# Kernel tuning notes

Hardware: AMD Instinct MI355X
Metric: run time of the kernel (lower is better)

The kernel has to match this reference:

```python
import jax, jax.numpy as jnp
import numpy as np

N_NODES = 30000
N_EDGES = 480000
NUM_RELS = 8
NUM_BASES = 4
F_IN = 32
HID = 64
HEADS = 4
N_CLASSES = 3
NEG_SLOPE = 0.2


def setup_inputs() -> dict:
    key = jax.random.key(0)
    ks = jax.random.split(key, 16)
    s = lambda k, shape: jax.random.normal(k, shape, jnp.float32) * 0.1
    return {
        'x': jax.random.normal(ks[0], (N_NODES, F_IN), jnp.float32),
        'edge_index': jax.random.randint(ks[1], (2, N_EDGES), 0, N_NODES),
        'edge_type': jax.random.randint(ks[2], (N_EDGES,), 0, NUM_RELS),
        # RGCN layer 1 (basis decomposition)
        'basis1': s(ks[3], (NUM_BASES, F_IN, HID)),
        'comp1': s(ks[4], (NUM_RELS, NUM_BASES)),
        'root1': s(ks[5], (F_IN, HID)),
        'brg1': jnp.zeros((HID,), jnp.float32),
        # GAT layer 1 (concat=True -> out dim HEADS*HID)
        'Wg1': s(ks[6], (HID, HEADS * HID)),
        'atts1': s(ks[7], (HEADS, HID)),
        'attd1': s(ks[8], (HEADS, HID)),
        'bg1': jnp.zeros((HEADS * HID,), jnp.float32),
        # RGCN layer 2
        'basis2': s(ks[9], (NUM_BASES, HEADS * HID, HID)),
        'comp2': s(ks[10], (NUM_RELS, NUM_BASES)),
        'root2': s(ks[11], (HEADS * HID, HID)),
        'brg2': jnp.zeros((HID,), jnp.float32),
        # GAT layer 2 (concat=False -> mean over heads, out dim N_CLASSES)
        'Wg2': s(ks[12], (HID, HEADS * N_CLASSES)),
        'atts2': s(ks[13], (HEADS, N_CLASSES)),
        'attd2': s(ks[14], (HEADS, N_CLASSES)),
        'bg2': jnp.zeros((N_CLASSES,), jnp.float32),
    }


def _rgcn(x, src, dst, etype, basis, comp, root, bias):
    # RGCNConv with basis decomposition, aggr='mean' (PyG default), root weight + bias.
    n = x.shape[0]
    w = jnp.einsum('rb,bio->rio', comp, basis)          # [R, in, out]
    xr = jnp.einsum('ni,rio->nro', x, w)                # [N, R, out]
    msg = xr[src, etype]                                # [E, out] gather per edge
    agg = jax.ops.segment_sum(msg, dst, num_segments=n)
    deg = jax.ops.segment_sum(jnp.ones((src.shape[0],), x.dtype), dst, num_segments=n)
    agg = agg / jnp.maximum(deg, 1.0)[:, None]          # mean over incoming edges
    return agg + x @ root + bias


def _gat(x, src, dst, w, att_s, att_d, bias, concat):
    # GATConv with self-loops (PyG default add_self_loops=True).
    n = x.shape[0]
    heads, c = att_s.shape
    loop = jnp.arange(n)
    s2 = jnp.concatenate([src, loop])
    d2 = jnp.concatenate([dst, loop])
    h = (x @ w).reshape(n, heads, c)                    # [N, H, C]
    a_s = jnp.einsum('nhc,hc->nh', h, att_s)
    a_d = jnp.einsum('nhc,hc->nh', h, att_d)
    e = jax.nn.leaky_relu(a_s[s2] + a_d[d2], NEG_SLOPE)  # [E2, H]
    emax = jax.ops.segment_max(e, d2, num_segments=n)    # stable softmax over in-edges
    p = jnp.exp(e - emax[d2])
    denom = jax.ops.segment_sum(p, d2, num_segments=n)
    alpha = p / denom[d2]
    out = jax.ops.segment_sum(alpha[:, :, None] * h[s2], d2, num_segments=n)  # [N, H, C]
    if concat:
        return out.reshape(n, heads * c) + bias
    return out.mean(axis=1) + bias


def reference(x, edge_index, edge_type, basis1, comp1, root1, brg1, Wg1, atts1, attd1, bg1, basis2, comp2, root2, brg2, Wg2, atts2, attd2, bg2):
    src, dst = edge_index[0], edge_index[1]
    h = jax.nn.elu(_rgcn(x, src, dst, edge_type, basis1, comp1, root1, brg1))
    h = jax.nn.elu(_gat(h, src, dst, Wg1, atts1, attd1, bg1, True))
    h = jax.nn.elu(_rgcn(h, src, dst, edge_type, basis2, comp2, root2, brg2))
    h = _gat(h, src, dst, Wg2, atts2, attd2, bg2, False)   # [N, n_classes]
    return jnp.tanh(h.mean(axis=1, keepdims=True))         # [N, 1]
```

## Files before the change

kernel.cpp:

```cpp
#include <hip/hip_runtime.h>
#include <cstdint>
#include <cstddef>

#define NN 30000
#define NE 480000

typedef __attribute__((ext_vector_type(8))) short short8v;
typedef __attribute__((ext_vector_type(4))) float f32x4;

__device__ __forceinline__ float leakyf(float x){ return x > 0.f ? x : 0.2f * x; }
__device__ __forceinline__ float eluf(float x){ return x > 0.f ? x : expm1f(x); }

__device__ __forceinline__ float bf2f(unsigned short u){
  return __uint_as_float(((unsigned)u) << 16);
}
__device__ __forceinline__ unsigned short f2bf(float f){
  unsigned x = __float_as_uint(f);
  unsigned r = (x + 0x7FFFu + ((x >> 16) & 1u)) >> 16;
  return (unsigned short)r;
}

struct F4 { float x, y, z, w; };

__device__ __forceinline__ F4 ld4(const float* p){
  float4 v = *(const float4*)p;
  return F4{v.x, v.y, v.z, v.w};
}

__device__ __forceinline__ float4 redeg16(float4 v){
  v.x += __shfl_xor(v.x, 16); v.y += __shfl_xor(v.y, 16);
  v.z += __shfl_xor(v.z, 16); v.w += __shfl_xor(v.w, 16);
  v.x += __shfl_xor(v.x, 32); v.y += __shfl_xor(v.y, 32);
  v.z += __shfl_xor(v.z, 32); v.w += __shfl_xor(v.w, 32);
  return v;
}


__global__ void zero2_kernel(int* __restrict__ a, int* __restrict__ b, int n){
  int i = blockIdx.x * blockDim.x + threadIdx.x;
  if (i < n){ a[i] = 0; b[i] = 0; }
}

__global__ void count_kernel(const int* __restrict__ dst, int* __restrict__ deg, int E){
  int i = blockIdx.x * blockDim.x + threadIdx.x;
  if (i < E) atomicAdd(&deg[dst[i]], 1);
}

__global__ void scan1_kernel(const int* __restrict__ deg, int* __restrict__ offs,
                             int* __restrict__ bsum){
  __shared__ int sh[256];
  int blk = blockIdx.x, t = threadIdx.x, i = blk * 256 + t;
  int v = (i < NN) ? deg[i] : 0;
  sh[t] = v; __syncthreads();
  for (int o = 1; o < 256; o <<= 1){
    int tv = (t >= o) ? sh[t - o] : 0;
    __syncthreads();
    sh[t] += tv;
    __syncthreads();
  }
  if (i < NN) offs[i + 1] = sh[t];
  if (t == 255) bsum[blk] = sh[255];
}

__global__ void scan2_kernel(int* __restrict__ bsum, int nb){
  __shared__ int sh[256];
  int t = threadIdx.x;
  int v = (t < nb) ? bsum[t] : 0;
  sh[t] = v; __syncthreads();
  for (int o = 1; o < 256; o <<= 1){
    int tv = (t >= o) ? sh[t - o] : 0;
    __syncthreads();
    sh[t] += tv;
    __syncthreads();
  }
  if (t < nb) bsum[t] = sh[t];
}

__global__ void scan3_kernel(const int* __restrict__ bsum, int* __restrict__ offs){
  int i = blockIdx.x * 256 + threadIdx.x;
  if (i == 0) offs[0] = 0;
  if (i < NN){
    int blk = i >> 8;
    int add = blk ? bsum[blk - 1] : 0;
    offs[i + 1] += add;
  }
}

__global__ void scatter_kernel(const int* __restrict__ src, const int* __restrict__ dst,
                               const int* __restrict__ et, const int* __restrict__ offs,
                               int* __restrict__ cursor, int* __restrict__ csr_src,
                               int* __restrict__ csr_et, int E){
  int i = blockIdx.x * blockDim.x + threadIdx.x;
  if (i < E){
    int d = dst[i];
    int pos = offs[d] + atomicAdd(&cursor[d], 1);
    csr_src[pos] = src[i];
    csr_et[pos]  = et[i];
  }
}


__global__ void wcat2_kernel(const float* __restrict__ basis2, const float* __restrict__ root2,
                             float* __restrict__ Wcat){
  int idx = blockIdx.x * 256 + threadIdx.x;
  if (idx >= 256 * 384) return;
  int k = idx / 384, col = idx - k * 384;
  float v = 0.f;
  if (col < 256){
    int b = col >> 6, c = col & 63;
    v = basis2[((size_t)b * 256 + k) * 64 + c];
  } else if (col < 320){
    v = root2[(size_t)k * 64 + (col - 256)];
  }
  Wcat[idx] = v;
}

__global__ void packB_kernel(const float* __restrict__ W, int ldw, int ksteps, int total,
                             unsigned short* __restrict__ Bhi, unsigned short* __restrict__ Blo){
  int idx = blockIdx.x * 256 + threadIdx.x;
  if (idx >= total) return;
  int lane = idx & 63;
  int rest = idx >> 6;
  int ks = rest % ksteps;
  int nf16 = rest / ksteps;
  int col = nf16 * 16 + (lane & 15);
  int kbase = ks * 32 + ((lane >> 4) << 3);
  size_t obase = (size_t)idx * 8;
  #pragma unroll
  for (int j = 0; j < 8; j++){
    float v = W[(size_t)(kbase + j) * ldw + col];
    unsigned short h = f2bf(v);
    float res = v - bf2f(h);
    Bhi[obase + j] = h;
    Blo[obase + j] = f2bf(res);
  }
}

__global__ void wa_kernel(const float* __restrict__ Wg1, const float* __restrict__ atts1,
                          const float* __restrict__ attd1, float* __restrict__ wa_s,
                          float* __restrict__ wa_d){
  int t = threadIdx.x;
  int k = t >> 2, h = t & 3;
  float s = 0.f, d = 0.f;
  const float* wr = Wg1 + (size_t)k * 256 + h * 64;
  const float* pa = atts1 + h * 64;
  const float* pb = attd1 + h * 64;
  #pragma unroll 8
  for (int c = 0; c < 64; c++){ s += wr[c] * pa[c]; d += wr[c] * pb[c]; }
  wa_s[k * 4 + h] = s;
  wa_d[k * 4 + h] = d;
}

__global__ void logits_kernel(const float* __restrict__ h1, const float* __restrict__ wa_s,
                              const float* __restrict__ wa_d, float* __restrict__ as_,
                              float* __restrict__ ad_){
  __shared__ float ws[256], wd[256];
  int t = threadIdx.x;
  ws[t] = wa_s[t];
  wd[t] = wa_d[t];
  __syncthreads();
  int idx = blockIdx.x * 256 + t;
  int n = idx >> 2, h = idx & 3;
  if (n >= NN) return;
  float s = 0.f, d = 0.f;
  const float* hr = h1 + (size_t)n * 64;
  #pragma unroll 4
  for (int k4 = 0; k4 < 16; k4++){
    float4 hv = *(const float4*)(hr + k4 * 4);
    s += hv.x * ws[(k4*4+0)*4+h] + hv.y * ws[(k4*4+1)*4+h]
       + hv.z * ws[(k4*4+2)*4+h] + hv.w * ws[(k4*4+3)*4+h];
    d += hv.x * wd[(k4*4+0)*4+h] + hv.y * wd[(k4*4+1)*4+h]
       + hv.z * wd[(k4*4+2)*4+h] + hv.w * wd[(k4*4+3)*4+h];
  }
  as_[n * 4 + h] = s;
  ad_[n * 4 + h] = d;
}


__global__ void agg1_kernel(const float* __restrict__ x, const float* __restrict__ comp,
                            const int* __restrict__ offs, const int* __restrict__ csr_src,
                            const int* __restrict__ csr_et, float* __restrict__ agg){
  int wid  = (blockIdx.x * blockDim.x + threadIdx.x) >> 6;
  int lane = threadIdx.x & 63;
  if (wid >= NN) return;
  int q = lane & 15, eg = lane >> 4;
  int c2 = q * 2;
  int n0 = offs[wid], n1 = offs[wid + 1];
  float a00 = 0.f, a01 = 0.f, a10 = 0.f, a11 = 0.f;
  float a20 = 0.f, a21 = 0.f, a30 = 0.f, a31 = 0.f;
  for (int k = n0 + eg; k < n1; k += 4){
    int s = csr_src[k], e = csr_et[k];
    float2 v = *(const float2*)(x + (size_t)s * 32 + c2);
    F4 cp = ld4(comp + (size_t)e * 4);
    a00 += cp.x * v.x; a01 += cp.x * v.y;
    a10 += cp.y * v.x; a11 += cp.y * v.y;
    a20 += cp.z * v.x; a21 += cp.z * v.y;
    a30 += cp.w * v.x; a31 += cp.w * v.y;
  }
  #pragma unroll
  for (int o = 16; o < 64; o <<= 1){
    a00 += __shfl_xor(a00, o); a01 += __shfl_xor(a01, o);
    a10 += __shfl_xor(a10, o); a11 += __shfl_xor(a11, o);
    a20 += __shfl_xor(a20, o); a21 += __shfl_xor(a21, o);
    a30 += __shfl_xor(a30, o); a31 += __shfl_xor(a31, o);
  }
  int dg = n1 - n0;
  float sc = 1.f / (float)(dg > 0 ? dg : 1);
  if (lane < 16){
    float* ar = agg + (size_t)wid * 128 + c2;
    *(float2*)(ar)      = make_float2(a00 * sc, a01 * sc);
    *(float2*)(ar + 32) = make_float2(a10 * sc, a11 * sc);
    *(float2*)(ar + 64) = make_float2(a20 * sc, a21 * sc);
    *(float2*)(ar + 96) = make_float2(a30 * sc, a31 * sc);
  }
}


template<int RPT, bool ELU>
__global__ __launch_bounds__(256) void gemmT_kernel(
    const float* __restrict__ A1, int lda1, int K1,
    const float* __restrict__ W1, int ldw1,
    const float* __restrict__ A2, int lda2, int K2,
    const float* __restrict__ W2, int ldw2,
    const float* __restrict__ bias,
    float* __restrict__ Y, int ldy,
    int nrows, int acgoff, int wcgoff)
{
  __shared__ float At[32][RPT * 16 + 4];
  __shared__ float Wl[32][68];
  int t = threadIdx.x;
  int tc = t & 15, tr = t >> 4;
  int cg = blockIdx.x;
  int nbase = blockIdx.y * (RPT * 16);
  float acc[RPT][4];
  #pragma unroll
  for (int j = 0; j < RPT; j++)
    #pragma unroll
    for (int i = 0; i < 4; i++) acc[j][i] = 0.f;

  for (int seg = 0; seg < 2; seg++){
    const float* A = seg ? A2 : A1;
    const float* W = seg ? W2 : W1;
    int lda = seg ? lda2 : lda1;
    int ldw = seg ? ldw2 : ldw1;
    int K   = seg ? K2 : K1;
    if (A == nullptr || K <= 0) continue;
    A += (size_t)cg * acgoff;
    W += (size_t)cg * wcgoff;
    for (int k0 = 0; k0 < K; k0 += 32){
      #pragma unroll
      for (int i = 0; i < 2; i++){
        int e = i * 256 + t;
        int kk = e >> 4, c4 = (e & 15) << 2;
        float4 v = make_float4(0.f, 0.f, 0.f, 0.f);
        if (k0 + kk < K) v = *(const float4*)(W + (size_t)(k0 + kk) * ldw + c4);
        *(float4*)&Wl[kk][c4] = v;
      }
      #pragma unroll
      for (int i = 0; i < RPT / 2; i++){
        int e = i * 256 + t;
        int r = e >> 3, c4 = (e & 7) << 2;
        int n = nbase + r;
        float4 v = make_float4(0.f, 0.f, 0.f, 0.f);
        if (n < nrows && k0 + c4 < K) v = *(const float4*)(A + (size_t)n * lda + k0 + c4);
        At[c4 + 0][r] = v.x;
        At[c4 + 1][r] = v.y;
        At[c4 + 2][r] = v.z;
        At[c4 + 3][r] = v.w;
      }
      __syncthreads();
      #pragma unroll 4
      for (int k = 0; k < 32; k++){
        float4 wv = *(const float4*)&Wl[k][tc * 4];
        const float* pw = (const float*)&wv;
        #pragma unroll
        for (int jj = 0; jj < RPT / 4; jj++){
          float4 av = *(const float4*)&At[k][tr * RPT + jj * 4];
          const float* pa = (const float*)&av;
          #pragma unroll
          for (int j = 0; j < 4; j++)
            #pragma unroll
            for (int i = 0; i < 4; i++)
              acc[jj * 4 + j][i] = fmaf(pa[j], pw[i], acc[jj * 4 + j][i]);
        }
      }
      __syncthreads();
    }
  }

  float b0 = 0.f, b1 = 0.f, b2 = 0.f, b3 = 0.f;
  if (bias){
    b0 = bias[cg * 64 + tc * 4 + 0];
    b1 = bias[cg * 64 + tc * 4 + 1];
    b2 = bias[cg * 64 + tc * 4 + 2];
    b3 = bias[cg * 64 + tc * 4 + 3];
  }
  #pragma unroll
  for (int j = 0; j < RPT; j++){
    int n = nbase + tr * RPT + j;
    if (n < nrows){
      float y0 = acc[j][0] + b0, y1 = acc[j][1] + b1;
      float y2 = acc[j][2] + b2, y3 = acc[j][3] + b3;
      if (ELU){ y0 = eluf(y0); y1 = eluf(y1); y2 = eluf(y2); y3 = eluf(y3); }
      *(float4*)(Y + (size_t)n * ldy + cg * 64 + tc * 4) = make_float4(y0, y1, y2, y3);
    }
  }
}


template<int KSTEPS, bool ELU, bool BIAS>
__global__ __launch_bounds__(256) void gemm_mfma_kernel(
    const float* __restrict__ A, int lda, int acgoff,
    const unsigned short* __restrict__ Bhi, const unsigned short* __restrict__ Blo,
    const float* __restrict__ bias, float* __restrict__ Y, int ldy)
{
  int t = threadIdx.x;
  int lane = t & 63, wv = t >> 6;
  int cg = blockIdx.x;
  int mbase = blockIdx.y * 256 + wv * 64;
  int fr = lane & 15;
  int ksub = (lane >> 4) << 3;
  const float* Ab = A + (size_t)cg * acgoff;
  f32x4 acc[4][4];
  #pragma unroll
  for (int mi = 0; mi < 4; mi++)
    #pragma unroll
    for (int ni = 0; ni < 4; ni++)
      acc[mi][ni] = (f32x4){0.f, 0.f, 0.f, 0.f};

  #pragma unroll
  for (int ks = 0; ks < KSTEPS; ks++){
    short8v ahi[4], alo[4];
    #pragma unroll
    for (int mi = 0; mi < 4; mi++){
      int r = mbase + mi * 16 + fr;
      float av[8];
      if (r < NN){
        float4 p0 = *(const float4*)(Ab + (size_t)r * lda + ks * 32 + ksub);
        float4 p1 = *(const float4*)(Ab + (size_t)r * lda + ks * 32 + ksub + 4);
        av[0] = p0.x; av[1] = p0.y; av[2] = p0.z; av[3] = p0.w;
        av[4] = p1.x; av[5] = p1.y; av[6] = p1.z; av[7] = p1.w;
      } else {
        #pragma unroll
        for (int j = 0; j < 8; j++) av[j] = 0.f;
      }
      #pragma unroll
      for (int j = 0; j < 8; j++){
        unsigned short h = f2bf(av[j]);
        float res = av[j] - bf2f(h);
        ahi[mi][j] = (short)h;
        alo[mi][j] = (short)f2bf(res);
      }
    }
    #pragma unroll
    for (int ni = 0; ni < 4; ni++){
      size_t boff = ((((size_t)(cg * 4 + ni)) * KSTEPS + ks) * 64 + lane) * 8;
      short8v bh = *(const short8v*)(Bhi + boff);
      short8v bl = *(const short8v*)(Blo + boff);
      #pragma unroll
      for (int mi = 0; mi < 4; mi++){
        acc[mi][ni] = __builtin_amdgcn_mfma_f32_16x16x32_bf16(ahi[mi], bh, acc[mi][ni], 0, 0, 0);
        acc[mi][ni] = __builtin_amdgcn_mfma_f32_16x16x32_bf16(ahi[mi], bl, acc[mi][ni], 0, 0, 0);
        acc[mi][ni] = __builtin_amdgcn_mfma_f32_16x16x32_bf16(alo[mi], bh, acc[mi][ni], 0, 0, 0);
      }
    }
  }
  int crow = (lane >> 4) << 2;
  #pragma unroll
  for (int mi = 0; mi < 4; mi++){
    #pragma unroll
    for (int reg = 0; reg < 4; reg++){
      int r = mbase + mi * 16 + crow + reg;
      if (r < NN){
        #pragma unroll
        for (int ni = 0; ni < 4; ni++){
          float y = acc[mi][ni][reg];
          if (BIAS) y += bias[cg * 64 + ni * 16 + fr];
          if (ELU)  y = eluf(y);
          Y[(size_t)r * ldy + cg * 64 + ni * 16 + fr] = y;
        }
      }
    }
  }
}


__global__ __launch_bounds__(256) void gemm_l3_fused_kernel(
    const float* __restrict__ A,
    const unsigned short* __restrict__ Bhi, const unsigned short* __restrict__ Blo,
    const float* __restrict__ comp2,
    unsigned short* __restrict__ xr, float* __restrict__ rootb)
{
  int t = threadIdx.x;
  int lane = t & 63, wv = t >> 6;
  int of = blockIdx.x;
  int mbase = blockIdx.y * 64 + wv * 16;
  int fr = lane & 15;
  int ksub = (lane >> 4) << 3;
  f32x4 acc[5];
  #pragma unroll
  for (int b = 0; b < 5; b++) acc[b] = (f32x4){0.f, 0.f, 0.f, 0.f};

  int ar = mbase + fr;
  bool arok = (ar < NN);
  for (int ks = 0; ks < 8; ks++){
    float av[8];
    if (arok){
      float4 p0 = *(const float4*)(A + (size_t)ar * 256 + ks * 32 + ksub);
      float4 p1 = *(const float4*)(A + (size_t)ar * 256 + ks * 32 + ksub + 4);
      av[0] = p0.x; av[1] = p0.y; av[2] = p0.z; av[3] = p0.w;
      av[4] = p1.x; av[5] = p1.y; av[6] = p1.z; av[7] = p1.w;
    } else {
      #pragma unroll
      for (int j = 0; j < 8; j++) av[j] = 0.f;
    }
    short8v ahi, alo;
    #pragma unroll
    for (int j = 0; j < 8; j++){
      unsigned short h = f2bf(av[j]);
      float res = av[j] - bf2f(h);
      ahi[j] = (short)h;
      alo[j] = (short)f2bf(res);
    }
    #pragma unroll
    for (int b = 0; b < 5; b++){
      int nig = b * 4 + of;
      size_t boff = (((size_t)nig * 8 + ks) * 64 + lane) * 8;
      short8v bh = *(const short8v*)(Bhi + boff);
      short8v bl = *(const short8v*)(Blo + boff);
      acc[b] = __builtin_amdgcn_mfma_f32_16x16x32_bf16(ahi, bh, acc[b], 0, 0, 0);
      acc[b] = __builtin_amdgcn_mfma_f32_16x16x32_bf16(ahi, bl, acc[b], 0, 0, 0);
      acc[b] = __builtin_amdgcn_mfma_f32_16x16x32_bf16(alo, bh, acc[b], 0, 0, 0);
    }
  }

  float cp[32];
  #pragma unroll
  for (int i = 0; i < 32; i++) cp[i] = comp2[i];
  int crow = (lane >> 4) << 2;
  int col = of * 16 + fr;
  #pragma unroll
  for (int reg = 0; reg < 4; reg++){
    int r = mbase + crow + reg;
    if (r >= NN) continue;
    float b0 = acc[0][reg], b1 = acc[1][reg], b2 = acc[2][reg], b3 = acc[3][reg];
    rootb[(size_t)r * 64 + col] = acc[4][reg];
    #pragma unroll
    for (int rr = 0; rr < 8; rr++){
      float m = cp[rr*4+0]*b0 + cp[rr*4+1]*b1 + cp[rr*4+2]*b2 + cp[rr*4+3]*b3;
      xr[((size_t)r * 8 + rr) * 64 + col] = f2bf(m);
    }
  }
}


__global__ void gat1_agg_kernel(const float* __restrict__ h1, const float* __restrict__ as_,
                                const float* __restrict__ ad_, const int* __restrict__ offs,
                                const int* __restrict__ csr_src, float* __restrict__ aggG){
  int wid  = (blockIdx.x * blockDim.x + threadIdx.x) >> 6;
  int lane = threadIdx.x & 63;
  if (wid >= NN) return;
  int n0 = offs[wid], n1 = offs[wid + 1];
  int h = lane & 3;
  float adn_s = ad_[wid * 4 + h];
  float m = leakyf(as_[wid * 4 + h] + adn_s);
  for (int k = n0 + (lane >> 2); k < n1; k += 16){
    int s = csr_src[k];
    m = fmaxf(m, leakyf(as_[s * 4 + h] + adn_s));
  }
  #pragma unroll
  for (int o = 4; o < 64; o <<= 1) m = fmaxf(m, __shfl_xor(m, o));
  float m0 = __shfl(m, 0), m1 = __shfl(m, 1), m2 = __shfl(m, 2), m3 = __shfl(m, 3);
  int q = lane & 15, eg = lane >> 4;
  F4 adn = ld4(ad_ + (size_t)wid * 4);
  float den0 = 0.f, den1 = 0.f, den2 = 0.f, den3 = 0.f;
  float4 ac0 = make_float4(0.f,0.f,0.f,0.f), ac1 = ac0, ac2 = ac0, ac3 = ac0;
  for (int k = n0 + eg; k < n1; k += 4){
    int s = csr_src[k];
    F4 a = ld4(as_ + (size_t)s * 4);
    float p0 = expf(leakyf(a.x + adn.x) - m0);
    float p1 = expf(leakyf(a.y + adn.y) - m1);
    float p2 = expf(leakyf(a.z + adn.z) - m2);
    float p3 = expf(leakyf(a.w + adn.w) - m3);
    den0 += p0; den1 += p1; den2 += p2; den3 += p3;
    float4 v = *(const float4*)(h1 + (size_t)s * 64 + q * 4);
    ac0.x += p0*v.x; ac0.y += p0*v.y; ac0.z += p0*v.z; ac0.w += p0*v.w;
    ac1.x += p1*v.x; ac1.y += p1*v.y; ac1.z += p1*v.z; ac1.w += p1*v.w;
    ac2.x += p2*v.x; ac2.y += p2*v.y; ac2.z += p2*v.z; ac2.w += p2*v.w;
    ac3.x += p3*v.x; ac3.y += p3*v.y; ac3.z += p3*v.z; ac3.w += p3*v.w;
  }
  #pragma unroll
  for (int o = 16; o < 64; o <<= 1){
    den0 += __shfl_xor(den0, o); den1 += __shfl_xor(den1, o);
    den2 += __shfl_xor(den2, o); den3 += __shfl_xor(den3, o);
  }
  ac0 = redeg16(ac0); ac1 = redeg16(ac1); ac2 = redeg16(ac2); ac3 = redeg16(ac3);
  F4 asn = ld4(as_ + (size_t)wid * 4);
  float ps0 = expf(leakyf(asn.x + adn.x) - m0);
  float ps1 = expf(leakyf(asn.y + adn.y) - m1);
  float ps2 = expf(leakyf(asn.z + adn.z) - m2);
  float ps3 = expf(leakyf(asn.w + adn.w) - m3);
  if (lane < 16){
    float4 v = *(const float4*)(h1 + (size_t)wid * 64 + q * 4);
    float i0 = 1.f / (den0 + ps0), i1 = 1.f / (den1 + ps1);
    float i2 = 1.f / (den2 + ps2), i3 = 1.f / (den3 + ps3);
    float* ag = aggG + (size_t)wid * 256 + q * 4;
    *(float4*)(ag)       = make_float4((ac0.x+ps0*v.x)*i0, (ac0.y+ps0*v.y)*i0, (ac0.z+ps0*v.z)*i0, (ac0.w+ps0*v.w)*i0);
    *(float4*)(ag + 64)  = make_float4((ac1.x+ps1*v.x)*i1, (ac1.y+ps1*v.y)*i1, (ac1.z+ps1*v.z)*i1, (ac1.w+ps1*v.w)*i1);
    *(float4*)(ag + 128) = make_float4((ac2.x+ps2*v.x)*i2, (ac2.y+ps2*v.y)*i2, (ac2.z+ps2*v.z)*i2, (ac2.w+ps2*v.w)*i2);
    *(float4*)(ag + 192) = make_float4((ac3.x+ps3*v.x)*i3, (ac3.y+ps3*v.y)*i3, (ac3.z+ps3*v.z)*i3, (ac3.w+ps3*v.w)*i3);
  }
}


__global__ void rgcn2_agg_kernel(const unsigned short* __restrict__ xr,
                                 const float* __restrict__ rootb,
                                 const float* __restrict__ bias, const int* __restrict__ offs,
                                 const int* __restrict__ csr_src, const int* __restrict__ csr_et,
                                 float* __restrict__ h3){
  int wid  = (blockIdx.x * blockDim.x + threadIdx.x) >> 6;
  int lane = threadIdx.x & 63;
  if (wid >= NN) return;
  int q = lane & 7, eg = lane >> 3;
  int n0 = offs[wid], n1 = offs[wid + 1];
  float a[8];
  #pragma unroll
  for (int j = 0; j < 8; j++) a[j] = 0.f;
  for (int k = n0 + eg; k < n1; k += 8){
    int s = csr_src[k], e = csr_et[k];
    short8v u = *(const short8v*)(xr + ((size_t)s * 8 + e) * 64 + q * 8);
    #pragma unroll
    for (int j = 0; j < 8; j++) a[j] += bf2f((unsigned short)u[j]);
  }
  #pragma unroll
  for (int o = 8; o < 64; o <<= 1){
    #pragma unroll
    for (int j = 0; j < 8; j++) a[j] += __shfl_xor(a[j], o);
  }
  int dg = n1 - n0;
  float sc = 1.f / (float)(dg > 0 ? dg : 1);
  if (lane < 8){
    const float* rb = rootb + (size_t)wid * 64 + q * 8;
    float4 r0 = *(const float4*)(rb);
    float4 r1 = *(const float4*)(rb + 4);
    float4 b0 = *(const float4*)(bias + q * 8);
    float4 b1 = *(const float4*)(bias + q * 8 + 4);
    float* hp = h3 + (size_t)wid * 64 + q * 8;
    *(float4*)(hp)     = make_float4(eluf(a[0]*sc + r0.x + b0.x), eluf(a[1]*sc + r0.y + b0.y),
                                     eluf(a[2]*sc + r0.z + b0.z), eluf(a[3]*sc + r0.w + b0.w));
    *(float4*)(hp + 4) = make_float4(eluf(a[4]*sc + r1.x + b1.x), eluf(a[5]*sc + r1.y + b1.y),
                                     eluf(a[6]*sc + r1.z + b1.z), eluf(a[7]*sc + r1.w + b1.w));
  }
}


__global__ void gat_lin2_kernel(const float* __restrict__ h, const float* __restrict__ W,
                                const float* __restrict__ atts, const float* __restrict__ attd,
                                float* __restrict__ hw, float* __restrict__ as_, float* __restrict__ ad_){
  int wid  = (blockIdx.x * blockDim.x + threadIdx.x) >> 6;
  int lane = threadIdx.x & 63;
  if (wid >= NN) return;
  float acc = 0.f;
  if (lane < 12){
    const float* hr = h + (size_t)wid * 64;
    const float* Wc = W + lane;
    #pragma unroll 8
    for (int i = 0; i < 64; i++) acc += hr[i] * Wc[(size_t)i * 12];
    hw[(size_t)wid * 12 + lane] = acc;
  }
  float ts = (lane < 12) ? acc * atts[lane] : 0.f;
  float td = (lane < 12) ? acc * attd[lane] : 0.f;
  int b = (lane < 4) ? lane * 3 : 0;
  float s0 = __shfl(ts, b) + __shfl(ts, b + 1) + __shfl(ts, b + 2);
  float d0 = __shfl(td, b) + __shfl(td, b + 1) + __shfl(td, b + 2);
  if (lane < 4){ as_[wid * 4 + lane] = s0; ad_[wid * 4 + lane] = d0; }
}

__global__ void gat2_final_kernel(const float* __restrict__ hw, const float* __restrict__ as_,
                                  const float* __restrict__ ad_, const float* __restrict__ bg2,
                                  const int* __restrict__ offs, const int* __restrict__ csr_src,
                                  float* __restrict__ out){
  int wid  = (blockIdx.x * blockDim.x + threadIdx.x) >> 6;
  int lane = threadIdx.x & 63;
  if (wid >= NN) return;
  int n0 = offs[wid], n1 = offs[wid + 1];
  F4 adn = ld4(ad_ + (size_t)wid * 4);
  F4 asn = ld4(as_ + (size_t)wid * 4);
  F4 es{leakyf(asn.x + adn.x), leakyf(asn.y + adn.y), leakyf(asn.z + adn.z), leakyf(asn.w + adn.w)};
  F4 m = es;
  for (int k = n0 + lane; k < n1; k += 64){
    int s = csr_src[k];
    F4 a = ld4(as_ + (size_t)s * 4);
    m.x = fmaxf(m.x, leakyf(a.x + adn.x));
    m.y = fmaxf(m.y, leakyf(a.y + adn.y));
    m.z = fmaxf(m.z, leakyf(a.z + adn.z));
    m.w = fmaxf(m.w, leakyf(a.w + adn.w));
  }
  #pragma unroll
  for (int o = 32; o; o >>= 1){
    m.x = fmaxf(m.x, __shfl_xor(m.x, o));
    m.y = fmaxf(m.y, __shfl_xor(m.y, o));
    m.z = fmaxf(m.z, __shfl_xor(m.z, o));
    m.w = fmaxf(m.w, __shfl_xor(m.w, o));
  }
  F4 ps{expf(es.x - m.x), expf(es.y - m.y), expf(es.z - m.z), expf(es.w - m.w)};
  float acc[12];
  #pragma unroll
  for (int j = 0; j < 12; j++) acc[j] = 0.f;
  F4 denp{0.f, 0.f, 0.f, 0.f};
  for (int k = n0 + lane; k < n1; k += 64){
    int s = csr_src[k];
    F4 a = ld4(as_ + (size_t)s * 4);
    F4 p{expf(leakyf(a.x + adn.x) - m.x), expf(leakyf(a.y + adn.y) - m.y),
         expf(leakyf(a.z + adn.z) - m.z), expf(leakyf(a.w + adn.w) - m.w)};
    denp.x += p.x; denp.y += p.y; denp.z += p.z; denp.w += p.w;
    const float* hb = hw + (size_t)s * 12;
    F4 h0 = ld4(hb), h1 = ld4(hb + 4), h2 = ld4(hb + 8);
    acc[0] += p.x * h0.x; acc[1]  += p.x * h0.y; acc[2]  += p.x * h0.z;
    acc[3] += p.y * h0.w; acc[4]  += p.y * h1.x; acc[5]  += p.y * h1.y;
    acc[6] += p.z * h1.z; acc[7]  += p.z * h1.w; acc[8]  += p.z * h2.x;
    acc[9] += p.w * h2.y; acc[10] += p.w * h2.z; acc[11] += p.w * h2.w;
  }
  #pragma unroll
  for (int o = 32; o; o >>= 1){
    denp.x += __shfl_xor(denp.x, o);
    denp.y += __shfl_xor(denp.y, o);
    denp.z += __shfl_xor(denp.z, o);
    denp.w += __shfl_xor(denp.w, o);
    #pragma unroll
    for (int j = 0; j < 12; j++) acc[j] += __shfl_xor(acc[j], o);
  }
  if (lane == 0){
    const float* hn = hw + (size_t)wid * 12;
    float dn[4]  = {denp.x + ps.x, denp.y + ps.y, denp.z + ps.z, denp.w + ps.w};
    float psv[4] = {ps.x, ps.y, ps.z, ps.w};
    float tot = 0.f;
    #pragma unroll
    for (int h_ = 0; h_ < 4; h_++){
      #pragma unroll
      for (int c = 0; c < 3; c++){
        float num = acc[h_ * 3 + c] + psv[h_] * hn[h_ * 3 + c];
        tot += num / dn[h_];
      }
    }
    tot = tot / 12.f + (bg2[0] + bg2[1] + bg2[2]) / 3.f;
    out[wid] = tanhf(tot);
  }
}


extern "C" void kernel_launch(void* const* d_in, const int* in_sizes, int n_in,
                              void* d_out, int out_size, void* d_ws, size_t ws_size,
                              hipStream_t stream){
  const float* x      = (const float*)d_in[0];
  const int*   ei     = (const int*)d_in[1];
  const int*   et     = (const int*)d_in[2];
  const float* basis1 = (const float*)d_in[3];
  const float* comp1  = (const float*)d_in[4];
  const float* root1  = (const float*)d_in[5];
  const float* brg1   = (const float*)d_in[6];
  const float* Wg1    = (const float*)d_in[7];
  const float* atts1  = (const float*)d_in[8];
  const float* attd1  = (const float*)d_in[9];
  const float* bg1    = (const float*)d_in[10];
  const float* basis2 = (const float*)d_in[11];
  const float* comp2  = (const float*)d_in[12];
  const float* root2  = (const float*)d_in[13];
  const float* brg2   = (const float*)d_in[14];
  const float* Wg2    = (const float*)d_in[15];
  const float* atts2  = (const float*)d_in[16];
  const float* attd2  = (const float*)d_in[17];
  const float* bg2    = (const float*)d_in[18];
  float* out = (float*)d_out;

  const int* src = ei;
  const int* dst = ei + NE;

  char* ws = (char*)d_ws;
  size_t off = 0;
  auto alloc = [&](size_t bytes) -> void* {
    void* p = ws + off;
    off = (off + bytes + 255) & ~(size_t)255;
    return p;
  };
  int*   deg     = (int*)alloc((size_t)NN * 4);
  int*   cursor  = (int*)alloc((size_t)NN * 4);
  int*   offs    = (int*)alloc((size_t)(NN + 1) * 4);
  int*   bsum    = (int*)alloc((size_t)256 * 4);
  int*   csr_src = (int*)alloc((size_t)NE * 4);
  int*   csr_et  = (int*)alloc((size_t)NE * 4);
  float* Wcat2   = (float*)alloc((size_t)256 * 384 * 4);
  unsigned short* Bhi2 = (unsigned short*)alloc((size_t)81920 * 2);
  unsigned short* Blo2 = (unsigned short*)alloc((size_t)81920 * 2);
  unsigned short* Bhi1 = (unsigned short*)alloc((size_t)16384 * 2);
  unsigned short* Blo1 = (unsigned short*)alloc((size_t)16384 * 2);
  float* wa_s    = (float*)alloc((size_t)256 * 4);
  float* wa_d    = (float*)alloc((size_t)256 * 4);
  float* h1      = (float*)alloc((size_t)NN * 64 * 4);
  float* h2      = (float*)alloc((size_t)NN * 256 * 4);
  float* h3      = (float*)alloc((size_t)NN * 64 * 4);
  float* hw2     = (float*)alloc((size_t)NN * 12 * 4);
  float* as1     = (float*)alloc((size_t)NN * 4 * 4);
  float* ad1     = (float*)alloc((size_t)NN * 4 * 4);
  float* as2     = (float*)alloc((size_t)NN * 4 * 4);
  float* ad2     = (float*)alloc((size_t)NN * 4 * 4);
  float* S       = (float*)alloc((size_t)NN * 384 * 4);
  float* agg1    = S;
  float* aggG    = S;
  unsigned short* xr = (unsigned short*)S;
  float* rootb   = S + (size_t)NN * 256;
  (void)ws_size; (void)n_in; (void)in_sizes; (void)out_size;

  const int BLK = 256;
  int gridN   = (NN + BLK - 1) / BLK;
  int gridE   = (NE + BLK - 1) / BLK;
  int gridW   = (NN + 3) / 4;
  int gridM64 = (NN + 63) / 64;
  int gridM256= (NN + 255) / 256;

  zero2_kernel<<<gridN, BLK, 0, stream>>>(deg, cursor, NN);
  count_kernel<<<gridE, BLK, 0, stream>>>(dst, deg, NE);
  wcat2_kernel<<<(256 * 384 + 255) / 256, BLK, 0, stream>>>(basis2, root2, Wcat2);
  packB_kernel<<<(10240 + 255) / 256, BLK, 0, stream>>>(Wcat2, 384, 8, 10240, Bhi2, Blo2);
  packB_kernel<<<(2048 + 255) / 256, BLK, 0, stream>>>(Wg1, 256, 2, 2048, Bhi1, Blo1);
  wa_kernel<<<1, BLK, 0, stream>>>(Wg1, atts1, attd1, wa_s, wa_d);
  scan1_kernel<<<gridN, BLK, 0, stream>>>(deg, offs, bsum);
  scan2_kernel<<<1, BLK, 0, stream>>>(bsum, gridN);
  scan3_kernel<<<gridN, BLK, 0, stream>>>(bsum, offs);
  scatter_kernel<<<gridE, BLK, 0, stream>>>(src, dst, et, offs, cursor, csr_src, csr_et, NE);

  agg1_kernel<<<gridW, BLK, 0, stream>>>(x, comp1, offs, csr_src, csr_et, agg1);
  gemmT_kernel<4, true><<<dim3(1, gridM64), BLK, 0, stream>>>(
      agg1, 128, 128, basis1, 64,
      x, 32, 32, root1, 64,
      brg1, h1, 64, NN, 0, 0);

  logits_kernel<<<(NN * 4 + 255) / 256, BLK, 0, stream>>>(h1, wa_s, wa_d, as1, ad1);
  gat1_agg_kernel<<<gridW, BLK, 0, stream>>>(h1, as1, ad1, offs, csr_src, aggG);
  gemm_mfma_kernel<2, true, true><<<dim3(4, gridM256), BLK, 0, stream>>>(
      aggG, 256, 64, Bhi1, Blo1, bg1, h2, 256);

  gemm_l3_fused_kernel<<<dim3(4, gridM64), BLK, 0, stream>>>(h2, Bhi2, Blo2, comp2, xr, rootb);
  rgcn2_agg_kernel<<<gridW, BLK, 0, stream>>>(xr, rootb, brg2, offs, csr_src, csr_et, h3);

  gat_lin2_kernel<<<gridW, BLK, 0, stream>>>(h3, Wg2, atts2, attd2, hw2, as2, ad2);
  gat2_final_kernel<<<gridW, BLK, 0, stream>>>(hw2, as2, ad2, bg2, offs, csr_src, out);
}
```

Baseline: 324.7 us.

## Fuse GAT logits into RGCN1 GEMM epilogue, merge weight packing, widen L3 tiles

The attention logit computation for GAT layer 1 moves into the epilogue of the first RGCN GEMM, using a 16-lane shuffle reduction. This drops a separate kernel launch and a re-read of h1. The concatenated-weight build and bf16 packing for layer 2 become one kernel, removing an intermediate buffer. The fused layer-3 MFMA GEMM now computes two 16-column output groups per block with half the grid, so each A-tile split into hi/lo bf16 is reused twice, at the cost of more accumulator registers.

Result: no change. 326.5 us (+0.5%).

```diff
diff --git a/kernel.cpp b/kernel.cpp
--- a/kernel.cpp
+++ b/kernel.cpp
@@ -100,19 +100,32 @@
 }
 
 
-__global__ void wcat2_kernel(const float* __restrict__ basis2, const float* __restrict__ root2,
-                             float* __restrict__ Wcat){
+__global__ void packB2_kernel(const float* __restrict__ basis2, const float* __restrict__ root2,
+                              unsigned short* __restrict__ Bhi, unsigned short* __restrict__ Blo){
   int idx = blockIdx.x * 256 + threadIdx.x;
-  if (idx >= 256 * 384) return;
-  int k = idx / 384, col = idx - k * 384;
-  float v = 0.f;
-  if (col < 256){
-    int b = col >> 6, c = col & 63;
-    v = basis2[((size_t)b * 256 + k) * 64 + c];
-  } else if (col < 320){
-    v = root2[(size_t)k * 64 + (col - 256)];
-  }
-  Wcat[idx] = v;
+  if (idx >= 10240) return;
+  int lane = idx & 63;
+  int rest = idx >> 6;
+  int ks = rest & 7;
+  int nf16 = rest >> 3;
+  int col = nf16 * 16 + (lane & 15);
+  int kbase = ks * 32 + ((lane >> 4) << 3);
+  size_t obase = (size_t)idx * 8;
+  #pragma unroll
+  for (int j = 0; j < 8; j++){
+    int k = kbase + j;
+    float v;
+    if (col < 256){
+      int b = col >> 6, c = col & 63;
+      v = basis2[((size_t)b * 256 + k) * 64 + c];
+    } else {
+      v = root2[(size_t)k * 64 + (col - 256)];
+    }
+    unsigned short h = f2bf(v);
+    float res = v - bf2f(h);
+    Bhi[obase + j] = h;
+    Blo[obase + j] = f2bf(res);
+  }
 }
 
 __global__ void packB_kernel(const float* __restrict__ W, int ldw, int ksteps, int total,
@@ -149,31 +162,6 @@
   for (int c = 0; c < 64; c++){ s += wr[c] * pa[c]; d += wr[c] * pb[c]; }
   wa_s[k * 4 + h] = s;
   wa_d[k * 4 + h] = d;
-}
-
-__global__ void logits_kernel(const float* __restrict__ h1, const float* __restrict__ wa_s,
-                              const float* __restrict__ wa_d, float* __restrict__ as_,
-                              float* __restrict__ ad_){
-  __shared__ float ws[256], wd[256];
-  int t = threadIdx.x;
-  ws[t] = wa_s[t];
-  wd[t] = wa_d[t];
-  __syncthreads();
-  int idx = blockIdx.x * 256 + t;
-  int n = idx >> 2, h = idx & 3;
-  if (n >= NN) return;
-  float s = 0.f, d = 0.f;
-  const float* hr = h1 + (size_t)n * 64;
-  #pragma unroll 4
-  for (int k4 = 0; k4 < 16; k4++){
-    float4 hv = *(const float4*)(hr + k4 * 4);
-    s += hv.x * ws[(k4*4+0)*4+h] + hv.y * ws[(k4*4+1)*4+h]
-       + hv.z * ws[(k4*4+2)*4+h] + hv.w * ws[(k4*4+3)*4+h];
-    d += hv.x * wd[(k4*4+0)*4+h] + hv.y * wd[(k4*4+1)*4+h]
-       + hv.z * wd[(k4*4+2)*4+h] + hv.w * wd[(k4*4+3)*4+h];
-  }
-  as_[n * 4 + h] = s;
-  ad_[n * 4 + h] = d;
 }
 
 
@@ -216,7 +204,7 @@
 }
 
 
-template<int RPT, bool ELU>
+template<int RPT, bool ELU, bool LOGITS>
 __global__ __launch_bounds__(256) void gemmT_kernel(
     const float* __restrict__ A1, int lda1, int K1,
     const float* __restrict__ W1, int ldw1,
@@ -224,14 +212,15 @@
     const float* __restrict__ W2, int ldw2,
     const float* __restrict__ bias,
     float* __restrict__ Y, int ldy,
-    int nrows, int acgoff, int wcgoff)
+    int nrows,
+    const float* __restrict__ wa_s, const float* __restrict__ wa_d,
+    float* __restrict__ as_, float* __restrict__ ad_)
 {
   __shared__ float At[32][RPT * 16 + 4];
   __shared__ float Wl[32][68];
   int t = threadIdx.x;
   int tc = t & 15, tr = t >> 4;
-  int cg = blockIdx.x;
-  int nbase = blockIdx.y * (RPT * 16);
+  int nbase = blockIdx.x * (RPT * 16);
   float acc[RPT][4];
   #pragma unroll
   for (int j = 0; j < RPT; j++)
@@ -245,8 +234,6 @@
     int ldw = seg ? ldw2 : ldw1;
     int K   = seg ? K2 : K1;
     if (A == nullptr || K <= 0) continue;
-    A += (size_t)cg * acgoff;
-    W += (size_t)cg * wcgoff;
     for (int k0 = 0; k0 < K; k0 += 32){
       #pragma unroll
       for (int i = 0; i < 2; i++){
@@ -288,21 +275,43 @@
     }
   }
 
-  float b0 = 0.f, b1 = 0.f, b2 = 0.f, b3 = 0.f;
-  if (bias){
-    b0 = bias[cg * 64 + tc * 4 + 0];
-    b1 = bias[cg * 64 + tc * 4 + 1];
-    b2 = bias[cg * 64 + tc * 4 + 2];
-    b3 = bias[cg * 64 + tc * 4 + 3];
+  float b0 = bias[tc * 4 + 0], b1 = bias[tc * 4 + 1];
+  float b2 = bias[tc * 4 + 2], b3 = bias[tc * 4 + 3];
+  float4 ws0, ws1, ws2, ws3, wd0, wd1, wd2, wd3;
+  if (LOGITS){
+    ws0 = *(const float4*)(wa_s + (tc*4+0)*4); wd0 = *(const float4*)(wa_d + (tc*4+0)*4);
+    ws1 = *(const float4*)(wa_s + (tc*4+1)*4); wd1 = *(const float4*)(wa_d + (tc*4+1)*4);
+    ws2 = *(const float4*)(wa_s + (tc*4+2)*4); wd2 = *(const float4*)(wa_d + (tc*4+2)*4);
+    ws3 = *(const float4*)(wa_s + (tc*4+3)*4); wd3 = *(const float4*)(wa_d + (tc*4+3)*4);
   }
   #pragma unroll
   for (int j = 0; j < RPT; j++){
     int n = nbase + tr * RPT + j;
-    if (n < nrows){
-      float y0 = acc[j][0] + b0, y1 = acc[j][1] + b1;
-      float y2 = acc[j][2] + b2, y3 = acc[j][3] + b3;
-      if (ELU){ y0 = eluf(y0); y1 = eluf(y1); y2 = eluf(y2); y3 = eluf(y3); }
-      *(float4*)(Y + (size_t)n * ldy + cg * 64 + tc * 4) = make_float4(y0, y1, y2, y3);
+    float y0 = acc[j][0] + b0, y1 = acc[j][1] + b1;
+    float y2 = acc[j][2] + b2, y3 = acc[j][3] + b3;
+    if (ELU){ y0 = eluf(y0); y1 = eluf(y1); y2 = eluf(y2); y3 = eluf(y3); }
+    if (n < nrows)
+      *(float4*)(Y + (size_t)n * ldy + tc * 4) = make_float4(y0, y1, y2, y3);
+    if (LOGITS){
+      float s0 = y0*ws0.x + y1*ws1.x + y2*ws2.x + y3*ws3.x;
+      float s1 = y0*ws0.y + y1*ws1.y + y2*ws2.y + y3*ws3.y;
+      float s2 = y0*ws0.z + y1*ws1.z + y2*ws2.z + y3*ws3.z;
+      float s3 = y0*ws0.w + y1*ws1.w + y2*ws2.w + y3*ws3.w;
+      float d0 = y0*wd0.x + y1*wd1.x + y2*wd2.x + y3*wd3.x;
+      float d1 = y0*wd0.y + y1*wd1.y + y2*wd2.y + y3*wd3.y;
+      float d2 = y0*wd0.z + y1*wd1.z + y2*wd2.z + y3*wd3.z;
+      float d3 = y0*wd0.w + y1*wd1.w + y2*wd2.w + y3*wd3.w;
+      #pragma unroll
+      for (int o = 1; o < 16; o <<= 1){
+        s0 += __shfl_xor(s0, o); s1 += __shfl_xor(s1, o);
+        s2 += __shfl_xor(s2, o); s3 += __shfl_xor(s3, o);
+        d0 += __shfl_xor(d0, o); d1 += __shfl_xor(d1, o);
+        d2 += __shfl_xor(d2, o); d3 += __shfl_xor(d3, o);
+      }
+      if (tc == 0 && n < nrows){
+        *(float4*)(as_ + n * 4) = make_float4(s0, s1, s2, s3);
+        *(float4*)(ad_ + n * 4) = make_float4(d0, d1, d2, d3);
+      }
     }
   }
 }
@@ -393,13 +402,15 @@
 {
   int t = threadIdx.x;
   int lane = t & 63, wv = t >> 6;
-  int of = blockIdx.x;
+  int of2 = blockIdx.x;
   int mbase = blockIdx.y * 64 + wv * 16;
   int fr = lane & 15;
   int ksub = (lane >> 4) << 3;
-  f32x4 acc[5];
-  #pragma unroll
-  for (int b = 0; b < 5; b++) acc[b] = (f32x4){0.f, 0.f, 0.f, 0.f};
+  f32x4 acc[2][5];
+  #pragma unroll
+  for (int o = 0; o < 2; o++)
+    #pragma unroll
+    for (int b = 0; b < 5; b++) acc[o][b] = (f32x4){0.f, 0.f, 0.f, 0.f};
 
   int ar = mbase + fr;
   bool arok = (ar < NN);
@@ -423,14 +434,17 @@
       alo[j] = (short)f2bf(res);
     }
     #pragma unroll
-    for (int b = 0; b < 5; b++){
-      int nig = b * 4 + of;
-      size_t boff = (((size_t)nig * 8 + ks) * 64 + lane) * 8;
-      short8v bh = *(const short8v*)(Bhi + boff);
-      short8v bl = *(const short8v*)(Blo + boff);
-      acc[b] = __builtin_amdgcn_mfma_f32_16x16x32_bf16(ahi, bh, acc[b], 0, 0, 0);
-      acc[b] = __builtin_amdgcn_mfma_f32_16x16x32_bf16(ahi, bl, acc[b], 0, 0, 0);
-      acc[b] = __builtin_amdgcn_mfma_f32_16x16x32_bf16(alo, bh, acc[b], 0, 0, 0);
+    for (int o = 0; o < 2; o++){
+      #pragma unroll
+      for (int b = 0; b < 5; b++){
+        int nig = b * 4 + of2 * 2 + o;
+        size_t boff = (((size_t)nig * 8 + ks) * 64 + lane) * 8;
+        short8v bh = *(const short8v*)(Bhi + boff);
+        short8v bl = *(const short8v*)(Blo + boff);
+        acc[o][b] = __builtin_amdgcn_mfma_f32_16x16x32_bf16(ahi, bh, acc[o][b], 0, 0, 0);
+        acc[o][b] = __builtin_amdgcn_mfma_f32_16x16x32_bf16(ahi, bl, acc[o][b], 0, 0, 0);
+        acc[o][b] = __builtin_amdgcn_mfma_f32_16x16x32_bf16(alo, bh, acc[o][b], 0, 0, 0);
+      }
     }
   }
 
@@ -438,17 +452,21 @@
   #pragma unroll
   for (int i = 0; i < 32; i++) cp[i] = comp2[i];
   int crow = (lane >> 4) << 2;
-  int col = of * 16 + fr;
   #pragma unroll
   for (int reg = 0; reg < 4; reg++){
     int r = mbase + crow + reg;
     if (r >= NN) continue;
-    float b0 = acc[0][reg], b1 = acc[1][reg], b2 = acc[2][reg], b3 = acc[3][reg];
-    rootb[(size_t)r * 64 + col] = acc[4][reg];
-    #pragma unroll
-    for (int rr = 0; rr < 8; rr++){
-      float m = cp[rr*4+0]*b0 + cp[rr*4+1]*b1 + cp[rr*4+2]*b2 + cp[rr*4+3]*b3;
-      xr[((size_t)r * 8 + rr) * 64 + col] = f2bf(m);
+    #pragma unroll
+    for (int o = 0; o < 2; o++){
+      int col = (of2 * 2 + o) * 16 + fr;
+      float b0 = acc[o][0][reg], b1 = acc[o][1][reg];
+      float b2 = acc[o][2][reg], b3 = acc[o][3][reg];
+      rootb[(size_t)r * 64 + col] = acc[o][4][reg];
+      #pragma unroll
+      for (int rr = 0; rr < 8; rr++){
+        float m = cp[rr*4+0]*b0 + cp[rr*4+1]*b1 + cp[rr*4+2]*b2 + cp[rr*4+3]*b3;
+        xr[((size_t)r * 8 + rr) * 64 + col] = f2bf(m);
+      }
     }
   }
 }
@@ -689,7 +707,6 @@
   int*   bsum    = (int*)alloc((size_t)256 * 4);
   int*   csr_src = (int*)alloc((size_t)NE * 4);
   int*   csr_et  = (int*)alloc((size_t)NE * 4);
-  float* Wcat2   = (float*)alloc((size_t)256 * 384 * 4);
   unsigned short* Bhi2 = (unsigned short*)alloc((size_t)81920 * 2);
   unsigned short* Blo2 = (unsigned short*)alloc((size_t)81920 * 2);
   unsigned short* Bhi1 = (unsigned short*)alloc((size_t)16384 * 2);
@@ -720,8 +737,7 @@
 
   zero2_kernel<<<gridN, BLK, 0, stream>>>(deg, cursor, NN);
   count_kernel<<<gridE, BLK, 0, stream>>>(dst, deg, NE);
-  wcat2_kernel<<<(256 * 384 + 255) / 256, BLK, 0, stream>>>(basis2, root2, Wcat2);
-  packB_kernel<<<(10240 + 255) / 256, BLK, 0, stream>>>(Wcat2, 384, 8, 10240, Bhi2, Blo2);
+  packB2_kernel<<<(10240 + 255) / 256, BLK, 0, stream>>>(basis2, root2, Bhi2, Blo2);
   packB_kernel<<<(2048 + 255) / 256, BLK, 0, stream>>>(Wg1, 256, 2, 2048, Bhi1, Blo1);
   wa_kernel<<<1, BLK, 0, stream>>>(Wg1, atts1, attd1, wa_s, wa_d);
   scan1_kernel<<<gridN, BLK, 0, stream>>>(deg, offs, bsum);
@@ -730,17 +746,16 @@
   scatter_kernel<<<gridE, BLK, 0, stream>>>(src, dst, et, offs, cursor, csr_src, csr_et, NE);
 
   agg1_kernel<<<gridW, BLK, 0, stream>>>(x, comp1, offs, csr_src, csr_et, agg1);
-  gemmT_kernel<4, true><<<dim3(1, gridM64), BLK, 0, stream>>>(
+  gemmT_kernel<4, true, true><<<gridM64, BLK, 0, stream>>>(
       agg1, 128, 128, basis1, 64,
       x, 32, 32, root1, 64,
-      brg1, h1, 64, NN, 0, 0);
-
-  logits_kernel<<<(NN * 4 + 255) / 256, BLK, 0, stream>>>(h1, wa_s, wa_d, as1, ad1);
+      brg1, h1, 64, NN, wa_s, wa_d, as1, ad1);
+
   gat1_agg_kernel<<<gridW, BLK, 0, stream>>>(h1, as1, ad1, offs, csr_src, aggG);
   gemm_mfma_kernel<2, true, true><<<dim3(4, gridM256), BLK, 0, stream>>>(
       aggG, 256, 64, Bhi1, Blo1, bg1, h2, 256);
 
-  gemm_l3_fused_kernel<<<dim3(4, gridM64), BLK, 0, stream>>>(h2, Bhi2, Blo2, comp2, xr, rootb);
+  gemm_l3_fused_kernel<<<dim3(2, gridM64), BLK, 0, stream>>>(h2, Bhi2, Blo2, comp2, xr, rootb);
   rgcn2_agg_kernel<<<gridW, BLK, 0, stream>>>(xr, rootb, brg2, offs, csr_src, csr_et, h3);
 
   gat_lin2_kernel<<<gridW, BLK, 0, stream>>>(h3, Wg2, atts2, attd2, hw2, as2, ad2);
```
